# Kernel tuning notes

Hardware: AMD Instinct MI355X
Metric: run time of the kernel (lower is better)

Reference implementation:

```python
import jax, jax.numpy as jnp
import numpy as np

N_NODES = 50000
N_EDGES = 1600000
IN_DIM = 128
OUT_DIM = 16
N_HEADS = 8


def setup_inputs() -> dict:
    key = jax.random.key(0)
    ks = jax.random.split(key, 9)
    s = 1.0 / np.sqrt(IN_DIM)
    return {
        "h": jax.random.normal(ks[0], (N_NODES, IN_DIM), jnp.float32),
        "Wq": jax.random.normal(ks[1], (IN_DIM, OUT_DIM * N_HEADS), jnp.float32) * s,
        "bq": jax.random.normal(ks[2], (OUT_DIM * N_HEADS,), jnp.float32) * 0.01,
        "Wk": jax.random.normal(ks[3], (IN_DIM, OUT_DIM * N_HEADS), jnp.float32) * s,
        "bk": jax.random.normal(ks[4], (OUT_DIM * N_HEADS,), jnp.float32) * 0.01,
        "Wv": jax.random.normal(ks[5], (IN_DIM, OUT_DIM * N_HEADS), jnp.float32) * s,
        "bv": jax.random.normal(ks[6], (OUT_DIM * N_HEADS,), jnp.float32) * 0.01,
        "src": jax.random.randint(ks[7], (N_EDGES,), 0, N_NODES, jnp.int32),
        "dst": jax.random.randint(ks[8], (N_EDGES,), 0, N_NODES, jnp.int32),
    }


def reference(h, Wq, bq, Wk, bk, Wv, bv, src, dst):
    n_nodes = h.shape[0]
    # node-wise Q/K/V projections -> [N, H, D]
    Q = (h @ Wq + bq).reshape(n_nodes, N_HEADS, OUT_DIM)
    K = (h @ Wk + bk).reshape(n_nodes, N_HEADS, OUT_DIM)
    V = (h @ Wv + bv).reshape(n_nodes, N_HEADS, OUT_DIM)
    # edge-wise score: (K[src] * Q[dst]).sum(-1), scaled-exp with clamp
    score = jnp.sum(K[src] * Q[dst], axis=-1)  # [E, H]
    score = jnp.exp(jnp.clip(score / np.sqrt(OUT_DIM), -5.0, 5.0))
    # scatter-sum weighted values and normalizers to dst nodes
    msg = V[src] * score[:, :, None]  # [E, H, D]
    wV = jax.ops.segment_sum(msg, dst, num_segments=n_nodes)  # [N, H, D]
    z = jax.ops.segment_sum(score, dst, num_segments=n_nodes)  # [N, H]
    return wV / (z[:, :, None] + 1e-6)
```

## Files before the change

### kernel.cpp

```cpp
#include <hip/hip_runtime.h>
#include <hip/hip_bf16.h>
#include <cstddef>

#define N_NODES 50000
#define N_EDGES 1600000
#define IN_DIM 128
#define OUT_DIM 16
#define N_HEADS 8
#define QKV_DIM 128
#define HS_STRIDE 136

#define SUBB 3125
#define BCAP 1024
#define BH_CHUNK 8192
#define BH_BLOCKS 196
#define GEMM_M 64
#define GEMM_BLOCKS 782
#define FUSED_BLOCKS (BH_BLOCKS + GEMM_BLOCKS)

typedef __hip_bfloat16 bf16;
typedef short bf16x8 __attribute__((ext_vector_type(8)));
typedef float f32x4  __attribute__((ext_vector_type(4)));

__device__ __forceinline__ float b2f(bf16 x) { return __bfloat162float(x); }

__device__ __forceinline__ float u16tof(unsigned int u) {
    unsigned int x = u << 16;
    float f;
    __builtin_memcpy(&f, &x, 4);
    return f;
}

__device__ __forceinline__ unsigned short f2bf(float v) {
    bf16 b = __float2bfloat16(v);
    unsigned short u;
    __builtin_memcpy(&u, &b, 2);
    return u;
}

__global__ __launch_bounds__(256) void sentinel_kernel(unsigned short* __restrict__ out, int n) {
    int i = blockIdx.x * 256 + threadIdx.x;
    if (i < n) out[i] = 0x42C8;
}

__global__ __launch_bounds__(256) void prep_kernel(
    const unsigned short* __restrict__ hraw,
    const void* __restrict__ Wqr, const void* __restrict__ bqr,
    const void* __restrict__ Wkr, const void* __restrict__ bkr,
    const void* __restrict__ Wvr, const void* __restrict__ bvr,
    int* __restrict__ flag,
    unsigned short* __restrict__ Wfrag, float* __restrict__ bias_f)
{
    __shared__ int red[256];
    const int t   = threadIdx.x;
    const int tid = blockIdx.x * 256 + t;

    int cnt = 0;
    for (int i = t; i < 8192; i += 256) {
        unsigned short u = hraw[i];
        int e = (u >> 7) & 0xFF;
        if (e == 0xFF || e > 0x85 || (e == 0 && (u & 0x7F) != 0)) cnt++;
    }
    red[t] = cnt;
    __syncthreads();
    for (int s = 128; s > 0; s >>= 1) {
        if (t < s) red[t] += red[t + s];
        __syncthreads();
    }
    const bool f32 = (red[0] > 100);
    if (blockIdx.x == 0 && t == 0) *flag = red[0];

    if (tid < 384) {
        int mat = tid >> 7, c = tid & 127;
        const void* bp = (mat == 0) ? bqr : (mat == 1) ? bkr : bvr;
        bias_f[tid] = f32 ? ((const float*)bp)[c] : b2f(((const bf16*)bp)[c]);
    }

    int l  = tid & 63;
    int s  = (tid >> 6) & 3;
    int nt = tid >> 8;
    int n  = nt * 16 + (l & 15);
    int k0 = s * 32 + (l >> 4) * 8;
    int mat = n >> 7, c = n & 127;
    const void* Wp = (mat == 0) ? Wqr : (mat == 1) ? Wkr : Wvr;

    unsigned short v[8];
#pragma unroll
    for (int j = 0; j < 8; ++j) {
        int k = k0 + j;
        float w = f32 ? ((const float*)Wp)[k * QKV_DIM + c]
                      : b2f(((const bf16*)Wp)[k * QKV_DIM + c]);
        v[j] = f2bf(w);
    }
    ushort4* o = (ushort4*)(Wfrag + (size_t)tid * 8);
    o[0] = make_ushort4(v[0], v[1], v[2], v[3]);
    o[1] = make_ushort4(v[4], v[5], v[6], v[7]);
}

__global__ __launch_bounds__(256) void fused_gs_kernel(
    const void* __restrict__ hraw,
    const unsigned short* __restrict__ Wfrag, const float* __restrict__ bias_f,
    const int* __restrict__ flag,
    unsigned short* __restrict__ Qt, unsigned short* __restrict__ KVt,
    const int* __restrict__ src, const int* __restrict__ dst,
    unsigned int* __restrict__ packed, unsigned int* __restrict__ offcnt)
{
    __shared__ __align__(16) unsigned char arena[GEMM_M * HS_STRIDE * 2];
    const int t = threadIdx.x;

    if (blockIdx.x < BH_BLOCKS) {
        int* lcnt = (int*)arena;
        int* sm   = (int*)(arena + 12544);

        const int b    = blockIdx.x;
        const int base = b * BH_CHUNK;
        const int nb   = min(N_EDGES - base, BH_CHUNK);

        for (int i = t; i < SUBB; i += 256) lcnt[i] = 0;
        __syncthreads();

        for (int i = t; i < nb; i += 256)
            atomicAdd(&lcnt[dst[base + i] >> 4], 1);
        __syncthreads();

        {
            const int lane = t & 63;
            const int wave = t >> 6;
            const int i0   = t * 13;

            int xs[13];
            int ssum = 0;
#pragma unroll
            for (int j = 0; j < 13; ++j) {
                int i = i0 + j;
                int x = (i < SUBB) ? lcnt[i] : 0;
                xs[j] = x;
                ssum += x;
            }
            int v = ssum;
#pragma unroll
            for (int sh = 1; sh < 64; sh <<= 1) {
                int a = __shfl_up(v, sh);
                if (lane >= sh) v += a;
            }
            if (lane == 63) sm[wave] = v;
            __syncthreads();
            int run = v - ssum;
#pragma unroll
            for (int w = 0; w < 4; ++w)
                if (w < wave) run += sm[w];
#pragma unroll
            for (int j = 0; j < 13; ++j) {
                int i = i0 + j;
                if (i < SUBB) {
                    offcnt[(size_t)b * SUBB + i] =
                        ((unsigned int)run << 16) | (unsigned int)xs[j];
                    lcnt[i] = run;
                    run += xs[j];
                }
            }
            __syncthreads();
        }

        for (int i = t; i < nb; i += 256) {
            int d = dst[base + i];
            int bk = d >> 4;
            int pos = atomicAdd(&lcnt[bk], 1);
            packed[base + pos] = (unsigned int)src[base + i] | ((unsigned int)(d & 15) << 16);
        }

    } else {
        unsigned short* smem = (unsigned short*)arena;

        const bool f32 = (*flag > 100);
        const int m0 = (blockIdx.x - BH_BLOCKS) * GEMM_M;

#pragma unroll
        for (int it = 0; it < 8; ++it) {
            int idx = it * 1024 + t * 4;
            int r = idx >> 7, k = idx & 127;
            int row = m0 + r;
            ushort4 w4 = make_ushort4(0, 0, 0, 0);
            if (row < N_NODES) {
                if (f32) {
                    float4 v4 = ((const float4*)hraw)[(size_t)row * 32 + (k >> 2)];
                    w4 = make_ushort4(f2bf(v4.x), f2bf(v4.y), f2bf(v4.z), f2bf(v4.w));
                } else {
                    uint2 u = ((const uint2*)hraw)[(size_t)row * 32 + (k >> 2)];
                    w4 = make_ushort4((unsigned short)(u.x & 0xffffu), (unsigned short)(u.x >> 16),
                                      (unsigned short)(u.y & 0xffffu), (unsigned short)(u.y >> 16));
                }
            }
            *(ushort4*)&smem[r * HS_STRIDE + k] = w4;
        }
        __syncthreads();

        const int lane = t & 63;
        const int wave = t >> 6;
        const int qd   = lane >> 4;
        const int ln15 = lane & 15;

        bf16x8 afr[4][4];
#pragma unroll
        for (int ms = 0; ms < 4; ++ms)
#pragma unroll
            for (int s = 0; s < 4; ++s)
                afr[ms][s] = *(const bf16x8*)&smem[(ms * 16 + ln15) * HS_STRIDE + s * 32 + qd * 8];

        __syncthreads();

#pragma unroll
        for (int p = 0; p < 3; ++p) {
#pragma unroll
            for (int ii = 0; ii < 2; ++ii) {
                const int i   = 2 * p + ii;
                const int nt  = wave + i * 4;
                const int col = nt * 16 + ln15;
                const float bs = bias_f[col];
                const int c127 = col & 127;

                bf16x8 bfr[4];
#pragma unroll
                for (int s = 0; s < 4; ++s)
                    bfr[s] = *(const bf16x8*)(Wfrag + ((size_t)(nt * 4 + s) * 64 + lane) * 8);

#pragma unroll
                for (int ms = 0; ms < 4; ++ms) {
                    f32x4 acc = {0.f, 0.f, 0.f, 0.f};
#pragma unroll
                    for (int s = 0; s < 4; ++s)
                        acc = __builtin_amdgcn_mfma_f32_16x16x32_bf16(afr[ms][s], bfr[s], acc, 0, 0, 0);
#pragma unroll
                    for (int r = 0; r < 4; ++r) {
                        int rl = ms * 16 + qd * 4 + r;
                        smem[rl * HS_STRIDE + c127] = f2bf(acc[r] + bs);
                    }
                }
            }
            __syncthreads();
            if (p == 0) {
                for (int q = t; q < 1024; q += 256) {
                    int row = q >> 4, c = q & 15;
                    int grow = m0 + row;
                    if (grow < N_NODES)
                        ((uint4*)Qt)[grow * 16 + c] = *(const uint4*)&smem[row * HS_STRIDE + c * 8];
                }
            } else {
                for (int q = t; q < 2048; q += 256) {
                    int row = q >> 5, g = q & 31;
                    int grow = m0 + row;
                    if (grow < N_NODES)
                        ((uint2*)KVt)[(size_t)grow * 64 + g * 2 + (p - 1)] =
                            *(const uint2*)&smem[row * HS_STRIDE + g * 4];
                }
            }
            __syncthreads();
        }
    }
}

__global__ __launch_bounds__(256, 8) void bucket_agg_kernel(
    const unsigned short* __restrict__ Qt, const unsigned short* __restrict__ KVt,
    const unsigned int* __restrict__ packed, const unsigned int* __restrict__ offcnt,
    const int* __restrict__ flag, void* __restrict__ out)
{
    __shared__ unsigned int   lds_pk[BCAP];
    __shared__ unsigned short lds_src[BCAP];
    __shared__ int runoff[BH_BLOCKS], runcnt[BH_BLOCKS], runpfx[BH_BLOCKS];
    __shared__ int cnt16[16], base16[16], cur16[16];
    __shared__ int wsum[4];
    __shared__ int nb_s;

    const int sb = blockIdx.x;
    const int t  = threadIdx.x;

    if (t < 16) { cnt16[t] = 0; cur16[t] = 0; }
    if (t < BH_BLOCKS) {
        unsigned int oc = offcnt[(size_t)t * SUBB + sb];
        runoff[t] = t * BH_CHUNK + (int)(oc >> 16);
        runcnt[t] = (int)(oc & 0xffffu);
    }
    __syncthreads();

    {
        const int lane = t & 63;
        const int wv   = t >> 6;
        int x = (t < BH_BLOCKS) ? runcnt[t] : 0;
        int v = x;
#pragma unroll
        for (int sh = 1; sh < 64; sh <<= 1) {
            int a = __shfl_up(v, sh);
            if (lane >= sh) v += a;
        }
        if (lane == 63) wsum[wv] = v;
        __syncthreads();
#pragma unroll
        for (int w = 0; w < 4; ++w)
            if (w < wv) v += wsum[w];
        if (t < BH_BLOCKS) runpfx[t] = v - x;
        if (t == 0) nb_s = wsum[0] + wsum[1] + wsum[2] + wsum[3];
        __syncthreads();
    }
    const int nb = min(nb_s, BCAP);

    for (int r = t; r < BH_BLOCKS; r += 256) {
        int ro = runoff[r], rc = runcnt[r], rp = runpfx[r];
        for (int j = 0; j < rc; ++j) {
            int dpos = rp + j;
            if (dpos < BCAP) {
                unsigned int pk = packed[ro + j];
                lds_pk[dpos] = pk;
                atomicAdd(&cnt16[(pk >> 16) & 15], 1);
            }
        }
    }
    __syncthreads();
    if (t == 0) {
        int acc = 0;
#pragma unroll
        for (int i = 0; i < 16; ++i) { base16[i] = acc; acc += cnt16[i]; }
    }
    __syncthreads();
    for (int j = t; j < nb; j += 256) {
        unsigned int pk = lds_pk[j];
        int dl = (pk >> 16) & 15;
        int pos = base16[dl] + atomicAdd(&cur16[dl], 1);
        lds_src[pos] = (unsigned short)(pk & 0xffffu);
    }
    __syncthreads();

    const int wave = t >> 6;
    const int lane = t & 63;
    const int half = lane >> 5;
    const int hl   = lane & 31;
    const uint4* KV4 = (const uint4*)KVt;
    const bool of32 = (*flag > 100);

    for (int dl = wave; dl < 16; dl += 4) {
        const int d = sb * 16 + dl;
        uint2 qw = ((const uint2*)Qt)[d * 32 + hl];
        const float q0 = u16tof(qw.x & 0xffffu), q1 = u16tof(qw.x >> 16);
        const float q2 = u16tof(qw.y & 0xffffu), q3 = u16tof(qw.y >> 16);
        const int off = base16[dl];
        const int nd  = cnt16[dl];

        float a0 = 0.f, a1 = 0.f, a2 = 0.f, a3 = 0.f, zz = 0.f;

#define CONSUME(KV, SCMASK)                                                     \
        {                                                                       \
            float p = fmaf(u16tof((KV).x & 0xffffu), q0,                        \
                      fmaf(u16tof((KV).x >> 16), q1,                            \
                      fmaf(u16tof((KV).y & 0xffffu), q2,                        \
                           u16tof((KV).y >> 16) * q3)));                        \
            p += __shfl_xor(p, 1);                                              \
            p += __shfl_xor(p, 2);                                              \
            float sc = __expf(__builtin_amdgcn_fmed3f(p * 0.25f, -5.f, 5.f));   \
            sc *= (SCMASK);                                                     \
            a0 = fmaf(u16tof((KV).z & 0xffffu), sc, a0);                        \
            a1 = fmaf(u16tof((KV).z >> 16),     sc, a1);                        \
            a2 = fmaf(u16tof((KV).w & 0xffffu), sc, a2);                        \
            a3 = fmaf(u16tof((KV).w >> 16),     sc, a3);                        \
            zz += sc;                                                           \
        }

        int j = 0;
        for (; j + 8 <= nd; j += 8) {
            int e[4];
#pragma unroll
            for (int u = 0; u < 4; ++u) e[u] = lds_src[off + j + 2 * u + half];
            uint4 kv[4];
#pragma unroll
            for (int u = 0; u < 4; ++u) kv[u] = KV4[e[u] * 32 + hl];
#pragma unroll
            for (int u = 0; u < 4; ++u) CONSUME(kv[u], 1.f)
        }
        for (; j + 2 <= nd; j += 2) {
            int e = lds_src[off + j + half];
            uint4 kv = KV4[e * 32 + hl];
            CONSUME(kv, 1.f)
        }
        if (j < nd) {
            int e = lds_src[off + j];
            uint4 kv = KV4[e * 32 + hl];
            CONSUME(kv, (half == 0) ? 1.f : 0.f)
        }
#undef CONSUME

        a0 += __shfl_xor(a0, 32);
        a1 += __shfl_xor(a1, 32);
        a2 += __shfl_xor(a2, 32);
        a3 += __shfl_xor(a3, 32);
        zz += __shfl_xor(zz, 32);

        const float inv = 1.f / (zz + 1e-6f);
        const float r0 = a0 * inv, r1 = a1 * inv, r2 = a2 * inv, r3 = a3 * inv;

        if (half == 0) {
            if (of32) {
                ((float4*)out)[d * 32 + hl] = make_float4(r0, r1, r2, r3);
            } else {
                unsigned int w0 = ((unsigned int)f2bf(r1) << 16) | f2bf(r0);
                unsigned int w1 = ((unsigned int)f2bf(r3) << 16) | f2bf(r2);
                ((uint2*)out)[d * 32 + hl] = make_uint2(w0, w1);
            }
        }
    }
}

extern "C" void kernel_launch(void* const* d_in, const int* in_sizes, int n_in,
                              void* d_out, int out_size, void* d_ws, size_t ws_size,
                              hipStream_t stream)
{
    const void* h  = d_in[0];
    const void* Wq = d_in[1];
    const void* bq = d_in[2];
    const void* Wk = d_in[3];
    const void* bk = d_in[4];
    const void* Wv = d_in[5];
    const void* bv = d_in[6];
    const int*  src = (const int*)d_in[7];
    const int*  dst = (const int*)d_in[8];

    const size_t NQ = (size_t)N_NODES * QKV_DIM;
    const size_t WFRAG_N = 24 * 4 * 64 * 8;
    const size_t PACKED_N = (size_t)BH_BLOCKS * BH_CHUNK;
    const size_t OFFCNT_N = (size_t)BH_BLOCKS * SUBB;

    const size_t need = 3 * NQ * 2 + WFRAG_N * 2 + 384 * 4 + 64
                      + PACKED_N * 4 + OFFCNT_N * 4;

    if (ws_size < need) {
        sentinel_kernel<<<(out_size + 255) / 256, 256, 0, stream>>>((unsigned short*)d_out, out_size);
        return;
    }

    unsigned short* Qt  = (unsigned short*)d_ws;
    unsigned short* KVt = Qt + NQ;
    unsigned short* Wfrag = KVt + 2 * NQ;
    float* bias_f = (float*)(Wfrag + WFRAG_N);
    int* flag     = (int*)(bias_f + 384);
    unsigned int* packed = (unsigned int*)(flag + 16);
    unsigned int* offcnt = packed + PACKED_N;

    prep_kernel<<<24, 256, 0, stream>>>((const unsigned short*)h,
        Wq, bq, Wk, bk, Wv, bv, flag, Wfrag, bias_f);

    fused_gs_kernel<<<FUSED_BLOCKS, 256, 0, stream>>>(h, Wfrag, bias_f, flag,
        Qt, KVt, src, dst, packed, offcnt);

    bucket_agg_kernel<<<SUBB, 256, 0, stream>>>(Qt, KVt, packed, offcnt, flag, d_out);
}
```

Measured before the change: 253.9 us.

## Use head-major Q/KV layout, split bucket sort, and parallelize aggregation per head

```diff
diff --git a/kernel.cpp b/kernel.cpp
--- a/kernel.cpp
+++ b/kernel.cpp
@@ -17,6 +17,7 @@
 #define GEMM_M 64
 #define GEMM_BLOCKS 782
 #define FUSED_BLOCKS (BH_BLOCKS + GEMM_BLOCKS)
+#define AGG_BLOCKS (SUBB * 8)
 
 typedef __hip_bfloat16 bf16;
 typedef short bf16x8 __attribute__((ext_vector_type(8)));
@@ -242,16 +243,22 @@
                 for (int q = t; q < 1024; q += 256) {
                     int row = q >> 4, c = q & 15;
                     int grow = m0 + row;
-                    if (grow < N_NODES)
-                        ((uint4*)Qt)[grow * 16 + c] = *(const uint4*)&smem[row * HS_STRIDE + c * 8];
+                    if (grow < N_NODES) {
+                        int head = c >> 1, half = c & 1;
+                        ((uint4*)Qt)[(size_t)head * (N_NODES * 2) + grow * 2 + half] =
+                            *(const uint4*)&smem[row * HS_STRIDE + c * 8];
+                    }
                 }
             } else {
                 for (int q = t; q < 2048; q += 256) {
                     int row = q >> 5, g = q & 31;
                     int grow = m0 + row;
-                    if (grow < N_NODES)
-                        ((uint2*)KVt)[(size_t)grow * 64 + g * 2 + (p - 1)] =
+                    if (grow < N_NODES) {
+                        int head = g >> 2, quart = g & 3;
+                        ((uint2*)KVt)[(size_t)head * (N_NODES * 8) + grow * 8
+                                      + ((p == 1) ? 0 : 4) + quart] =
                             *(const uint2*)&smem[row * HS_STRIDE + g * 4];
+                    }
                 }
             }
             __syncthreads();
@@ -259,10 +266,9 @@
     }
 }
 
-__global__ __launch_bounds__(256, 8) void bucket_agg_kernel(
-    const unsigned short* __restrict__ Qt, const unsigned short* __restrict__ KVt,
+__global__ __launch_bounds__(256) void sortbk_kernel(
     const unsigned int* __restrict__ packed, const unsigned int* __restrict__ offcnt,
-    const int* __restrict__ flag, void* __restrict__ out)
+    unsigned short* __restrict__ gsorted, int* __restrict__ gcnt)
 {
     __shared__ unsigned int   lds_pk[BCAP];
     __shared__ unsigned short lds_src[BCAP];
@@ -329,79 +335,116 @@
     }
     __syncthreads();
 
+    for (int j = t; j < nb; j += 256)
+        gsorted[(size_t)sb * BCAP + j] = lds_src[j];
+    if (t < 16) gcnt[sb * 16 + t] = cnt16[t];
+}
+
+__global__ __launch_bounds__(256) void bucket_agg_kernel(
+    const unsigned short* __restrict__ QH, const unsigned short* __restrict__ KVH,
+    const unsigned short* __restrict__ gsorted, const int* __restrict__ gcnt,
+    const int* __restrict__ flag, void* __restrict__ out)
+{
+    __shared__ unsigned short lds_src[BCAP];
+    __shared__ int cnt16[16], base16[16];
+    __shared__ int tot_s;
+
+    const int sb = blockIdx.x >> 3;
+    const int hh = blockIdx.x & 7;
+    const int t  = threadIdx.x;
+
+    if (t < 16) cnt16[t] = gcnt[sb * 16 + t];
+    __syncthreads();
+    if (t == 0) {
+        int acc = 0;
+#pragma unroll
+        for (int i = 0; i < 16; ++i) { base16[i] = acc; acc += cnt16[i]; }
+        tot_s = acc;
+    }
+    __syncthreads();
+    const int total = tot_s;
+    for (int j = t; j < total; j += 256)
+        lds_src[j] = __builtin_nontemporal_load(&gsorted[(size_t)sb * BCAP + j]);
+    __syncthreads();
+
     const int wave = t >> 6;
     const int lane = t & 63;
-    const int half = lane >> 5;
-    const int hl   = lane & 31;
-    const uint4* KV4 = (const uint4*)KVt;
+    const int g4   = lane >> 2;
+    const int u    = lane & 3;
     const bool of32 = (*flag > 100);
+
+    const uint4* KV4 = (const uint4*)KVH;
+    const unsigned int* QW = (const unsigned int*)QH;
+    const size_t kvbase = (size_t)hh * (N_NODES * 4);
+    const size_t qwbase = (size_t)hh * (N_NODES * 8);
 
     for (int dl = wave; dl < 16; dl += 4) {
         const int d = sb * 16 + dl;
-        uint2 qw = ((const uint2*)Qt)[d * 32 + hl];
-        const float q0 = u16tof(qw.x & 0xffffu), q1 = u16tof(qw.x >> 16);
-        const float q2 = u16tof(qw.y & 0xffffu), q3 = u16tof(qw.y >> 16);
+
+        const unsigned int* qp = QW + qwbase + (size_t)d * 8 + (u & 1) * 4;
+        unsigned int qw0 = __builtin_nontemporal_load(qp + 0);
+        unsigned int qw1 = __builtin_nontemporal_load(qp + 1);
+        unsigned int qw2 = __builtin_nontemporal_load(qp + 2);
+        unsigned int qw3 = __builtin_nontemporal_load(qp + 3);
+        float qf[8];
+        qf[0] = u16tof(qw0 & 0xffffu); qf[1] = u16tof(qw0 >> 16);
+        qf[2] = u16tof(qw1 & 0xffffu); qf[3] = u16tof(qw1 >> 16);
+        qf[4] = u16tof(qw2 & 0xffffu); qf[5] = u16tof(qw2 >> 16);
+        qf[6] = u16tof(qw3 & 0xffffu); qf[7] = u16tof(qw3 >> 16);
+
         const int off = base16[dl];
         const int nd  = cnt16[dl];
 
-        float a0 = 0.f, a1 = 0.f, a2 = 0.f, a3 = 0.f, zz = 0.f;
-
-#define CONSUME(KV, SCMASK)                                                     \
-        {                                                                       \
-            float p = fmaf(u16tof((KV).x & 0xffffu), q0,                        \
-                      fmaf(u16tof((KV).x >> 16), q1,                            \
-                      fmaf(u16tof((KV).y & 0xffffu), q2,                        \
-                           u16tof((KV).y >> 16) * q3)));                        \
-            p += __shfl_xor(p, 1);                                              \
-            p += __shfl_xor(p, 2);                                              \
-            float sc = __expf(__builtin_amdgcn_fmed3f(p * 0.25f, -5.f, 5.f));   \
-            sc *= (SCMASK);                                                     \
-            a0 = fmaf(u16tof((KV).z & 0xffffu), sc, a0);                        \
-            a1 = fmaf(u16tof((KV).z >> 16),     sc, a1);                        \
-            a2 = fmaf(u16tof((KV).w & 0xffffu), sc, a2);                        \
-            a3 = fmaf(u16tof((KV).w >> 16),     sc, a3);                        \
-            zz += sc;                                                           \
-        }
-
-        int j = 0;
-        for (; j + 8 <= nd; j += 8) {
-            int e[4];
-#pragma unroll
-            for (int u = 0; u < 4; ++u) e[u] = lds_src[off + j + 2 * u + half];
-            uint4 kv[4];
-#pragma unroll
-            for (int u = 0; u < 4; ++u) kv[u] = KV4[e[u] * 32 + hl];
-#pragma unroll
-            for (int u = 0; u < 4; ++u) CONSUME(kv[u], 1.f)
-        }
-        for (; j + 2 <= nd; j += 2) {
-            int e = lds_src[off + j + half];
-            uint4 kv = KV4[e * 32 + hl];
-            CONSUME(kv, 1.f)
-        }
-        if (j < nd) {
-            int e = lds_src[off + j];
-            uint4 kv = KV4[e * 32 + hl];
-            CONSUME(kv, (half == 0) ? 1.f : 0.f)
-        }
-#undef CONSUME
-
-        a0 += __shfl_xor(a0, 32);
-        a1 += __shfl_xor(a1, 32);
-        a2 += __shfl_xor(a2, 32);
-        a3 += __shfl_xor(a3, 32);
-        zz += __shfl_xor(zz, 32);
+        float a[8] = {0.f, 0.f, 0.f, 0.f, 0.f, 0.f, 0.f, 0.f};
+        float zz = 0.f;
+
+        for (int j = 0; j < nd; j += 16) {
+            const int ei = j + g4;
+            const float msk = (ei < nd) ? 1.f : 0.f;
+            const int e = (ei < nd) ? (int)lds_src[off + ei] : 0;
+            uint4 kv = KV4[kvbase + (size_t)e * 4 + u];
+            float kf[8];
+            kf[0] = u16tof(kv.x & 0xffffu); kf[1] = u16tof(kv.x >> 16);
+            kf[2] = u16tof(kv.y & 0xffffu); kf[3] = u16tof(kv.y >> 16);
+            kf[4] = u16tof(kv.z & 0xffffu); kf[5] = u16tof(kv.z >> 16);
+            kf[6] = u16tof(kv.w & 0xffffu); kf[7] = u16tof(kv.w >> 16);
+
+            float pp = 0.f;
+#pragma unroll
+            for (int i = 0; i < 8; ++i) pp = fmaf(kf[i], qf[i], pp);
+            pp = (u < 2) ? pp : 0.f;
+            pp += __shfl_xor(pp, 1);
+            pp += __shfl_xor(pp, 2);
+            float sc = __expf(__builtin_amdgcn_fmed3f(pp * 0.25f, -5.f, 5.f)) * msk;
+#pragma unroll
+            for (int i = 0; i < 8; ++i) a[i] = fmaf(kf[i], sc, a[i]);
+            zz += sc;
+        }
+
+#pragma unroll
+        for (int s = 4; s <= 32; s <<= 1) {
+#pragma unroll
+            for (int i = 0; i < 8; ++i) a[i] += __shfl_xor(a[i], s);
+            zz += __shfl_xor(zz, s);
+        }
 
         const float inv = 1.f / (zz + 1e-6f);
-        const float r0 = a0 * inv, r1 = a1 * inv, r2 = a2 * inv, r3 = a3 * inv;
-
-        if (half == 0) {
+
+        if (g4 == 0 && u >= 2) {
+            const int dbase = (u - 2) * 8;
             if (of32) {
-                ((float4*)out)[d * 32 + hl] = make_float4(r0, r1, r2, r3);
+                float* op = (float*)out + (size_t)d * 128 + hh * 16 + dbase;
+#pragma unroll
+                for (int i = 0; i < 8; ++i)
+                    __builtin_nontemporal_store(a[i] * inv, op + i);
             } else {
-                unsigned int w0 = ((unsigned int)f2bf(r1) << 16) | f2bf(r0);
-                unsigned int w1 = ((unsigned int)f2bf(r3) << 16) | f2bf(r2);
-                ((uint2*)out)[d * 32 + hl] = make_uint2(w0, w1);
+                unsigned int* op = (unsigned int*)out + (size_t)d * 64 + hh * 8 + (u - 2) * 4;
+#pragma unroll
+                for (int i = 0; i < 4; ++i) {
+                    unsigned int w = ((unsigned int)f2bf(a[2 * i + 1] * inv) << 16)
+                                   | f2bf(a[2 * i] * inv);
+                    __builtin_nontemporal_store(w, op + i);
+                }
             }
         }
     }
@@ -425,9 +468,11 @@
     const size_t WFRAG_N = 24 * 4 * 64 * 8;
     const size_t PACKED_N = (size_t)BH_BLOCKS * BH_CHUNK;
     const size_t OFFCNT_N = (size_t)BH_BLOCKS * SUBB;
+    const size_t GS_N   = (size_t)SUBB * BCAP;
+    const size_t GCNT_N = (size_t)SUBB * 16;
 
     const size_t need = 3 * NQ * 2 + WFRAG_N * 2 + 384 * 4 + 64
-                      + PACKED_N * 4 + OFFCNT_N * 4;
+                      + PACKED_N * 4 + OFFCNT_N * 4 + GS_N * 2 + GCNT_N * 4;
 
     if (ws_size < need) {
         sentinel_kernel<<<(out_size + 255) / 256, 256, 0, stream>>>((unsigned short*)d_out, out_size);
@@ -441,6 +486,8 @@
     int* flag     = (int*)(bias_f + 384);
     unsigned int* packed = (unsigned int*)(flag + 16);
     unsigned int* offcnt = packed + PACKED_N;
+    unsigned short* gsorted = (unsigned short*)(offcnt + OFFCNT_N);
+    int* gcnt = (int*)(gsorted + GS_N);
 
     prep_kernel<<<24, 256, 0, stream>>>((const unsigned short*)h,
         Wq, bq, Wk, bk, Wv, bv, flag, Wfrag, bias_f);
@@ -448,5 +495,8 @@
     fused_gs_kernel<<<FUSED_BLOCKS, 256, 0, stream>>>(h, Wfrag, bias_f, flag,
         Qt, KVt, src, dst, packed, offcnt);
 
-    bucket_agg_kernel<<<SUBB, 256, 0, stream>>>(Qt, KVt, packed, offcnt, flag, d_out);
-}
+    sortbk_kernel<<<SUBB, 256, 0, stream>>>(packed, offcnt, gsorted, gcnt);
+
+    bucket_agg_kernel<<<AGG_BLOCKS, 256, 0, stream>>>(Qt, KVt, gsorted, gcnt,
+        flag, d_out);
+}
```

New measurement: 352.5 us. 1.39x slower.
